# Optimization experiments

Measured on AMD Instinct MI355X. Metric: run time of the kernel, lower is better.

## Reference

```python
import jax, jax.numpy as jnp
import numpy as np

D_MODEL = 4096
D_FIBER = 16
D_CONTROL = 64
EMA_MOMENTUM = 0.9


def setup_inputs() -> dict:
    key = jax.random.key(0)
    k_h, k_f, k_w1, k_w2 = jax.random.split(key, 4)
    B, S = 4, 2048
    hidden = jax.random.normal(k_h, (B, S, D_MODEL), dtype=jnp.float32)
    # torch nn.Linear stores weight as [out, in]; fiber_proj init: normal std=0.02
    W_fiber = jax.random.normal(k_f, (D_FIBER, D_MODEL), dtype=jnp.float32) * 0.02
    # predictor[0]: Linear(d_model+d_fiber, d_control) with default torch init (uniform)
    fan_in1 = D_MODEL + D_FIBER
    bound1 = 1.0 / np.sqrt(fan_in1)
    W1 = jax.random.uniform(k_w1, (D_CONTROL, fan_in1), dtype=jnp.float32, minval=-bound1, maxval=bound1)
    b1 = jnp.zeros((D_CONTROL,), dtype=jnp.float32)
    # predictor[-2]: Linear(d_control, 1), weight normal std=0.01, bias zero
    W2 = jax.random.normal(k_w2, (1, D_CONTROL), dtype=jnp.float32) * 0.01
    b2 = jnp.zeros((1,), dtype=jnp.float32)
    lam = jnp.asarray(1.0, dtype=jnp.float32)
    return {"hidden": hidden, "W_fiber": W_fiber, "W1": W1, "b1": b1, "W2": W2, "b2": b2, "lam": lam}


def _causal_ema(delta_h, alpha):
    # h_t = alpha*h_{t-1} + (1-alpha)*d_t, h_{-1} = 0. delta_h: [B,S]
    B = delta_h.shape[0]
    def step(h_prev, d_t):
        h_t = alpha * h_prev + (1.0 - alpha) * d_t
        return h_t, h_t
    _, hs = jax.lax.scan(step, jnp.zeros((B,), delta_h.dtype), jnp.swapaxes(delta_h, 0, 1))
    return jnp.swapaxes(hs, 0, 1)  # [B,S]


def reference(hidden, W_fiber, W1, b1, W2, b2, lam):
    h = hidden.astype(jnp.float32)                      # [B,S,D]
    fiber = jnp.einsum('bsd,fd->bsf', h, W_fiber)       # [B,S,16]
    combined = jnp.concatenate([h, fiber], axis=-1)     # [B,S,D+16]
    z = jax.nn.gelu(jnp.einsum('bsc,kc->bsk', combined, W1) + b1, approximate=False)
    delta_h = jax.nn.softplus(jnp.einsum('bsk,ok->bso', z, W2) + b2)[..., 0]  # [B,S]
    field = _causal_ema(delta_h, EMA_MOMENTUM)          # [B,S]
    gate = jax.nn.sigmoid(-lam * field)
    return gate.astype(hidden.dtype), field.astype(hidden.dtype), delta_h.mean()
```

## Files before the change

kernel.cpp:

```cpp
#include <hip/hip_runtime.h>
#include <hip/hip_bf16.h>

#define D_MODEL 4096
#define NTOK    8192
#define SEQ     2048
#define RS      264

typedef short bf16x8 __attribute__((ext_vector_type(8)));
typedef float f32x4  __attribute__((ext_vector_type(4)));

typedef const __attribute__((address_space(1))) char* gas1_t;
typedef __attribute__((address_space(3))) char* las3_t;

__device__ inline void async16(const void* g, void* l) {
  __builtin_amdgcn_global_load_lds((gas1_t)g, (las3_t)l, 16, 0, 0);
}

__device__ inline short f2bf(float x) {
  __hip_bfloat16 h = __float2bfloat16(x);
  return *reinterpret_cast<short*>(&h);
}
__device__ inline float bf2f(const void* p, size_t i) {
  return __bfloat162float(((const __hip_bfloat16*)p)[i]);
}

__global__ __launch_bounds__(320) void sniff_k(const void* hid, const void* wf,
                                               const void* w1, const void* w2,
                                               const void* b1, const void* b2,
                                               const void* lam,
                                               int* flags, float* scal) {
  int wv = threadIdx.x >> 6, lane = threadIdx.x & 63;
  const unsigned short* p = nullptr;
  int n = 0;
  switch (wv) {
    case 0: p = (const unsigned short*)hid; n = NTOK * D_MODEL; break;
    case 1: p = (const unsigned short*)wf;  n = 16 * D_MODEL;   break;
    case 2: p = (const unsigned short*)w1;  n = 64 * 4112;      break;
    case 3: p = (const unsigned short*)w2;  n = 64;             break;
    case 4: p = (const unsigned short*)b1;  n = 64;             break;
  }
  int S = n / 2 < 64 ? n / 2 : 64;
  bool act = lane < S;
  unsigned short ve = 0, vo = 0;
  if (act) { ve = p[2 * lane]; vo = p[2 * lane + 1]; }
  int ee = (ve >> 7) & 0xFF, eo = (vo >> 7) & 0xFF;
  bool ve_band   = (ve == 0) || (ve == 0x8000) || (ee >= 96 && ee <= 141);
  bool vo_bandnz = (vo != 0) && (vo != 0x8000) && (eo >= 96 && eo <= 141);
  int zp = __popcll(__ballot(act && ve == 0 && vo == 0));
  int ob = __popcll(__ballot(act && ve == 0 && vo_bandnz));
  int eb = __popcll(__ballot(act && ve_band));
  if (lane == 0) {
    int f;
    if (zp == S) f = 1;
    else if (4 * ob >= 3 * S) f = 0;
    else if (4 * eb >= 3 * S) f = 1;
    else f = 0;
    flags[wv] = f;
  }
  if (threadIdx.x == 0) {
    unsigned short l0 = *(const unsigned short*)lam;
    int le = (l0 >> 7) & 0xFF;
    if (l0 != 0 && l0 != 0x8000 && le >= 96 && le <= 141)
      scal[0] = __bfloat162float(*(const __hip_bfloat16*)lam);
    else
      scal[0] = *(const float*)lam;
    unsigned short c0 = *(const unsigned short*)b2;
    int ce = (c0 >> 7) & 0xFF;
    if (c0 == 0) scal[1] = 0.0f;
    else if (c0 != 0x8000 && ce >= 96 && ce <= 141)
      scal[1] = __bfloat162float(*(const __hip_bfloat16*)b2);
    else
      scal[1] = *(const float*)b2;
  }
}

__global__ __launch_bounds__(256) void fold_w1(const void* __restrict__ W1v,
                                               const void* __restrict__ Wfv,
                                               const int* __restrict__ flags,
                                               __hip_bfloat16* __restrict__ W1eff) {
  int n = blockIdx.x;
  int fw1 = flags[2], fwf = flags[1];
  __shared__ float w1b[16];
  if (threadIdx.x < 16) {
    size_t idx = (size_t)n * 4112 + 4096 + threadIdx.x;
    w1b[threadIdx.x] = fw1 ? bf2f(W1v, idx) : ((const float*)W1v)[idx];
  }
  __syncthreads();
  for (int k = threadIdx.x; k < D_MODEL; k += 256) {
    size_t idx = (size_t)n * 4112 + k;
    float v = fw1 ? bf2f(W1v, idx) : ((const float*)W1v)[idx];
#pragma unroll
    for (int f = 0; f < 16; ++f) {
      size_t wi = (size_t)f * D_MODEL + k;
      float wfv = fwf ? bf2f(Wfv, wi) : ((const float*)Wfv)[wi];
      v += w1b[f] * wfv;
    }
    W1eff[(size_t)n * D_MODEL + k] = __float2bfloat16(v);
  }
}

__global__ __launch_bounds__(256) void gemm_fused(const void* __restrict__ hid,
                                                  const short* __restrict__ B_,
                                                  const void* __restrict__ b1,
                                                  const void* __restrict__ w2,
                                                  const int* __restrict__ flags,
                                                  const float* __restrict__ scal,
                                                  float* __restrict__ delta) {
  __shared__ short As[2][32 * RS];
  __shared__ short Bs[2][64 * RS];
  int t = blockIdx.x;
  int tid = threadIdx.x;
  int w = tid >> 6, lane = tid & 63;
  int m = lane & 15, kg = lane >> 4;
  int kh = w >> 1, rg = w & 1;
  bool lo = lane < 32;
  int l5 = lane & 31;
  f32x4 acc[4];
#pragma unroll
  for (int g = 0; g < 4; ++g) acc[g] = (f32x4){0.f, 0.f, 0.f, 0.f};

  auto compute = [&](const short* Asc, const short* Bsc) {
#pragma unroll
    for (int j = 0; j < 4; ++j) {
      int ko = kh * 128 + j * 32 + kg * 8;
      bf16x8 a   = *(const bf16x8*)(Asc + (rg * 16 + m) * RS + ko);
      bf16x8 b0v = *(const bf16x8*)(Bsc + (m +  0) * RS + ko);
      bf16x8 b1v = *(const bf16x8*)(Bsc + (m + 16) * RS + ko);
      bf16x8 b2v = *(const bf16x8*)(Bsc + (m + 32) * RS + ko);
      bf16x8 b3v = *(const bf16x8*)(Bsc + (m + 48) * RS + ko);
      acc[0] = __builtin_amdgcn_mfma_f32_16x16x32_bf16(a, b0v, acc[0], 0, 0, 0);
      acc[1] = __builtin_amdgcn_mfma_f32_16x16x32_bf16(a, b1v, acc[1], 0, 0, 0);
      acc[2] = __builtin_amdgcn_mfma_f32_16x16x32_bf16(a, b2v, acc[2], 0, 0, 0);
      acc[3] = __builtin_amdgcn_mfma_f32_16x16x32_bf16(a, b3v, acc[3], 0, 0, 0);
    }
  };

  if (flags[0]) {
    const short* hidA = (const short*)hid;
    auto stage = [&](int c, int p) {
#pragma unroll
      for (int i = 0; i < 8; ++i) {
        int r = w * 8 + i;
        const short* gp = hidA + (size_t)(t * 32 + r) * D_MODEL + c * 256 + l5 * 8;
        if (lo) async16(gp, &As[p][r * RS]);
      }
#pragma unroll
      for (int i = 0; i < 16; ++i) {
        int r = w * 16 + i;
        const short* gp = B_ + (size_t)r * D_MODEL + c * 256 + l5 * 8;
        if (lo) async16(gp, &Bs[p][r * RS]);
      }
    };
    stage(0, 0);
#pragma unroll 1
    for (int c = 0; c < 15; ++c) {
      stage(c + 1, (c + 1) & 1);
      __builtin_amdgcn_s_waitcnt(0x4F78);
      __builtin_amdgcn_s_barrier();
      compute(As[c & 1], Bs[c & 1]);
      __builtin_amdgcn_s_barrier();
    }
    __builtin_amdgcn_s_waitcnt(0x0F70);
    __builtin_amdgcn_s_barrier();
    compute(As[1], Bs[1]);
  } else {
    const float* hidF = (const float*)hid;
#pragma unroll 1
    for (int c = 0; c < 16; ++c) {
#pragma unroll
      for (int i = 0; i < 16; ++i) {
        int r = w * 16 + i;
        const short* gp = B_ + (size_t)r * D_MODEL + c * 256 + l5 * 8;
        if (lo) async16(gp, &Bs[0][r * RS]);
      }
      for (int e = tid; e < 32 * 256; e += 256) {
        int r = e >> 8, k = e & 255;
        As[0][r * RS + k] = f2bf(hidF[(size_t)(t * 32 + r) * D_MODEL + c * 256 + k]);
      }
      __syncthreads();
      compute(As[0], Bs[0]);
      __syncthreads();
    }
  }

  float* red = (float*)&As[0][0];
#pragma unroll
  for (int g = 0; g < 4; ++g)
#pragma unroll
    for (int r = 0; r < 4; ++r)
      red[kh * 2048 + (rg * 16 + kg * 4 + r) * 64 + g * 16 + m] = acc[g][r];
  __syncthreads();
  int row = tid >> 3, cid = tid & 7;
  int fb1 = flags[4], fw2 = flags[3];
  float y = 0.f;
#pragma unroll
  for (int j = 0; j < 8; ++j) {
    int col = cid + 8 * j;
    float s = red[row * 64 + col] + red[2048 + row * 64 + col];
    s += fb1 ? bf2f(b1, col) : ((const float*)b1)[col];
    float gg = 0.5f * s * (1.0f + erff(s * 0.70710678118654752f));
    y += gg * (fw2 ? bf2f(w2, col) : ((const float*)w2)[col]);
  }
#pragma unroll
  for (int off = 1; off <= 4; off <<= 1) y += __shfl_xor(y, off, 64);
  if (cid == 0) {
    float x = y + scal[1];
    delta[t * 32 + row] = (x > 20.0f) ? x : log1pf(expf(x));
  }
}

__global__ __launch_bounds__(256) void ema_out(const float* __restrict__ delta,
                                               const float* __restrict__ scal,
                                               float* __restrict__ out) {
  int b    = threadIdx.x >> 6;
  int lane = threadIdx.x & 63;
  const float alpha = 0.9f;
  float d[32];
  const float* dp = delta + b * SEQ + lane * 32;
  float beta = 0.f, lsum = 0.f;
#pragma unroll
  for (int i = 0; i < 32; ++i) {
    d[i] = dp[i];
    lsum += d[i];
    beta = alpha * beta + 0.1f * d[i];
  }
  float accA = 0.03433683820292512f;
  float accB = beta;
  for (int off = 1; off < 64; off <<= 1) {
    float uA = __shfl_up(accA, off, 64);
    float uB = __shfl_up(accB, off, 64);
    if (lane >= off) {
      accB = accB + accA * uB;
      accA = accA * uA;
    }
  }
  float prev = __shfl_up(accB, 1, 64);
  float h = (lane == 0) ? 0.f : prev;
  float lam = scal[0];
#pragma unroll
  for (int i = 0; i < 32; ++i) {
    h = alpha * h + 0.1f * d[i];
    float gate = 1.0f / (1.0f + expf(lam * h));
    out[b * SEQ + lane * 32 + i]        = gate;
    out[NTOK + b * SEQ + lane * 32 + i] = h;
  }
#pragma unroll
  for (int off = 32; off >= 1; off >>= 1) lsum += __shfl_xor(lsum, off, 64);
  __shared__ float bs[4];
  if (lane == 0) bs[b] = lsum;
  __syncthreads();
  if (threadIdx.x == 0)
    out[2 * NTOK] = (bs[0] + bs[1] + bs[2] + bs[3]) * (1.0f / 8192.0f);
}

extern "C" void kernel_launch(void* const* d_in, const int* in_sizes, int n_in,
                              void* d_out, int out_size, void* d_ws, size_t ws_size,
                              hipStream_t stream) {
  const void* hidden = d_in[0];
  const void* Wf     = d_in[1];
  const void* W1     = d_in[2];
  const void* b1     = d_in[3];
  const void* W2     = d_in[4];
  const void* b2     = d_in[5];
  const void* lam    = d_in[6];
  float* out = (float*)d_out;

  char* ws = (char*)d_ws;
  int*   flags = (int*)ws;
  float* scal  = (float*)(ws + 32);
  __hip_bfloat16* W1eff = (__hip_bfloat16*)(ws + 64);
  float* delta = (float*)(ws + 64 + (size_t)64 * D_MODEL * 2);

  sniff_k<<<1, 320, 0, stream>>>(hidden, Wf, W1, W2, b1, b2, lam, flags, scal);
  fold_w1<<<64, 256, 0, stream>>>(W1, Wf, flags, W1eff);
  gemm_fused<<<256, 256, 0, stream>>>(hidden, (const short*)W1eff, b1, W2, flags, scal, delta);
  ema_out<<<1, 256, 0, stream>>>(delta, scal, out);
}
```

Baseline: 249.5 us.

## Split GEMM K dimension across four blocks with swizzled LDS and separate epilogue

The fused GEMM is split into a split-K partial kernel: 1024 blocks of 512 threads, each covering a quarter of K. Each block writes its partial 64-wide sums to workspace. A new small kernel reduces the partials and applies bias, GELU, the W2 dot product and softplus. LDS uses an XOR-swizzled layout without padding in place of the padded stride, and double buffering is dropped in favour of higher occupancy. This raises parallelism on a 256-CU device where only one block per CU ran before, at the cost of an extra launch and partial-sum traffic.

```diff
diff --git a/kernel.cpp b/kernel.cpp
--- a/kernel.cpp
+++ b/kernel.cpp
@@ -4,7 +4,6 @@
 #define D_MODEL 4096
 #define NTOK    8192
 #define SEQ     2048
-#define RS      264
 
 typedef short bf16x8 __attribute__((ext_vector_type(8)));
 typedef float f32x4  __attribute__((ext_vector_type(4)));
@@ -99,113 +98,116 @@
   }
 }
 
-__global__ __launch_bounds__(256) void gemm_fused(const void* __restrict__ hid,
-                                                  const short* __restrict__ B_,
-                                                  const void* __restrict__ b1,
-                                                  const void* __restrict__ w2,
-                                                  const int* __restrict__ flags,
-                                                  const float* __restrict__ scal,
-                                                  float* __restrict__ delta) {
-  __shared__ short As[2][32 * RS];
-  __shared__ short Bs[2][64 * RS];
-  int t = blockIdx.x;
+__global__ __launch_bounds__(512, 6) void gemm_part(const void* __restrict__ hid,
+                                                    const short* __restrict__ B_,
+                                                    const int* __restrict__ flags,
+                                                    float* __restrict__ part) {
+  __shared__ short SMEM[24576];
+  short* As = SMEM;
+  short* Bs = SMEM + 8192;
+  int t = blockIdx.x >> 2;
+  int q = blockIdx.x & 3;
   int tid = threadIdx.x;
   int w = tid >> 6, lane = tid & 63;
   int m = lane & 15, kg = lane >> 4;
-  int kh = w >> 1, rg = w & 1;
-  bool lo = lane < 32;
-  int l5 = lane & 31;
+  int rg = w & 1, kq = w >> 1;
+  int rdma = lane >> 5;
+  int sdma = lane & 31;
   f32x4 acc[4];
 #pragma unroll
   for (int g = 0; g < 4; ++g) acc[g] = (f32x4){0.f, 0.f, 0.f, 0.f};
 
-  auto compute = [&](const short* Asc, const short* Bsc) {
-#pragma unroll
-    for (int j = 0; j < 4; ++j) {
-      int ko = kh * 128 + j * 32 + kg * 8;
-      bf16x8 a   = *(const bf16x8*)(Asc + (rg * 16 + m) * RS + ko);
-      bf16x8 b0v = *(const bf16x8*)(Bsc + (m +  0) * RS + ko);
-      bf16x8 b1v = *(const bf16x8*)(Bsc + (m + 16) * RS + ko);
-      bf16x8 b2v = *(const bf16x8*)(Bsc + (m + 32) * RS + ko);
-      bf16x8 b3v = *(const bf16x8*)(Bsc + (m + 48) * RS + ko);
+  const short* hidA = (const short*)hid;
+  int fhid = flags[0];
+
+#pragma unroll 1
+  for (int c = 0; c < 4; ++c) {
+    int kbase = q * 1024 + c * 256;
+    if (fhid) {
+#pragma unroll
+      for (int i = 0; i < 2; ++i) {
+        int r0 = w * 4 + i * 2;
+        int r  = r0 + rdma;
+        const short* gp = hidA + (size_t)(t * 32 + r) * D_MODEL + kbase +
+                          ((sdma ^ (r & 7)) * 8);
+        async16(gp, As + r0 * 256);
+      }
+    } else {
+      for (int e = tid; e < 32 * 256; e += 512) {
+        int r = e >> 8, k = e & 255;
+        float v = ((const float*)hid)[(size_t)(t * 32 + r) * D_MODEL + kbase + k];
+        As[r * 256 + (((k >> 3) ^ (r & 7)) * 8) + (k & 7)] = f2bf(v);
+      }
+    }
+#pragma unroll
+    for (int i = 0; i < 4; ++i) {
+      int r0 = w * 8 + i * 2;
+      int r  = r0 + rdma;
+      const short* gp = B_ + (size_t)r * D_MODEL + kbase + ((sdma ^ (r & 7)) * 8);
+      async16(gp, Bs + r0 * 256);
+    }
+    __syncthreads();
+#pragma unroll
+    for (int j = 0; j < 2; ++j) {
+      int sl  = kq * 8 + j * 4 + kg;
+      int off = ((sl ^ (m & 7)) * 8);
+      bf16x8 a   = *(const bf16x8*)(As + (rg * 16 + m) * 256 + off);
+      bf16x8 b0v = *(const bf16x8*)(Bs + (m +  0) * 256 + off);
+      bf16x8 b1v = *(const bf16x8*)(Bs + (m + 16) * 256 + off);
+      bf16x8 b2v = *(const bf16x8*)(Bs + (m + 32) * 256 + off);
+      bf16x8 b3v = *(const bf16x8*)(Bs + (m + 48) * 256 + off);
       acc[0] = __builtin_amdgcn_mfma_f32_16x16x32_bf16(a, b0v, acc[0], 0, 0, 0);
       acc[1] = __builtin_amdgcn_mfma_f32_16x16x32_bf16(a, b1v, acc[1], 0, 0, 0);
       acc[2] = __builtin_amdgcn_mfma_f32_16x16x32_bf16(a, b2v, acc[2], 0, 0, 0);
       acc[3] = __builtin_amdgcn_mfma_f32_16x16x32_bf16(a, b3v, acc[3], 0, 0, 0);
     }
-  };
-
-  if (flags[0]) {
-    const short* hidA = (const short*)hid;
-    auto stage = [&](int c, int p) {
-#pragma unroll
-      for (int i = 0; i < 8; ++i) {
-        int r = w * 8 + i;
-        const short* gp = hidA + (size_t)(t * 32 + r) * D_MODEL + c * 256 + l5 * 8;
-        if (lo) async16(gp, &As[p][r * RS]);
-      }
-#pragma unroll
-      for (int i = 0; i < 16; ++i) {
-        int r = w * 16 + i;
-        const short* gp = B_ + (size_t)r * D_MODEL + c * 256 + l5 * 8;
-        if (lo) async16(gp, &Bs[p][r * RS]);
-      }
-    };
-    stage(0, 0);
-#pragma unroll 1
-    for (int c = 0; c < 15; ++c) {
-      stage(c + 1, (c + 1) & 1);
-      __builtin_amdgcn_s_waitcnt(0x4F78);
-      __builtin_amdgcn_s_barrier();
-      compute(As[c & 1], Bs[c & 1]);
-      __builtin_amdgcn_s_barrier();
-    }
-    __builtin_amdgcn_s_waitcnt(0x0F70);
-    __builtin_amdgcn_s_barrier();
-    compute(As[1], Bs[1]);
-  } else {
-    const float* hidF = (const float*)hid;
-#pragma unroll 1
-    for (int c = 0; c < 16; ++c) {
-#pragma unroll
-      for (int i = 0; i < 16; ++i) {
-        int r = w * 16 + i;
-        const short* gp = B_ + (size_t)r * D_MODEL + c * 256 + l5 * 8;
-        if (lo) async16(gp, &Bs[0][r * RS]);
-      }
-      for (int e = tid; e < 32 * 256; e += 256) {
-        int r = e >> 8, k = e & 255;
-        As[0][r * RS + k] = f2bf(hidF[(size_t)(t * 32 + r) * D_MODEL + c * 256 + k]);
-      }
-      __syncthreads();
-      compute(As[0], Bs[0]);
-      __syncthreads();
-    }
-  }
-
-  float* red = (float*)&As[0][0];
+    __syncthreads();
+  }
+
+  float* red = (float*)SMEM;
 #pragma unroll
   for (int g = 0; g < 4; ++g)
 #pragma unroll
     for (int r = 0; r < 4; ++r)
-      red[kh * 2048 + (rg * 16 + kg * 4 + r) * 64 + g * 16 + m] = acc[g][r];
+      red[((kq * 32) + (rg * 16 + kg * 4 + r)) * 64 + (g * 16 + m)] = acc[g][r];
   __syncthreads();
-  int row = tid >> 3, cid = tid & 7;
+  int row = tid >> 4, cid = tid & 15;
+  float* po = part + ((size_t)q * NTOK + (size_t)t * 32 + row) * 64;
+#pragma unroll
+  for (int j = 0; j < 4; ++j) {
+    int col = cid + 16 * j;
+    float s = red[(0 * 32 + row) * 64 + col] + red[(1 * 32 + row) * 64 + col] +
+              red[(2 * 32 + row) * 64 + col] + red[(3 * 32 + row) * 64 + col];
+    po[col] = s;
+  }
+}
+
+__global__ __launch_bounds__(256) void delta_ep(const float* __restrict__ part,
+                                                const void* __restrict__ b1,
+                                                const void* __restrict__ w2,
+                                                const int* __restrict__ flags,
+                                                const float* __restrict__ scal,
+                                                float* __restrict__ delta) {
+  int tok = blockIdx.x * 16 + (threadIdx.x >> 4);
+  int cid = threadIdx.x & 15;
   int fb1 = flags[4], fw2 = flags[3];
   float y = 0.f;
 #pragma unroll
-  for (int j = 0; j < 8; ++j) {
-    int col = cid + 8 * j;
-    float s = red[row * 64 + col] + red[2048 + row * 64 + col];
+  for (int j = 0; j < 4; ++j) {
+    int col = cid + 16 * j;
+    float s = 0.f;
+#pragma unroll
+    for (int c = 0; c < 4; ++c)
+      s += part[((size_t)c * NTOK + tok) * 64 + col];
     s += fb1 ? bf2f(b1, col) : ((const float*)b1)[col];
-    float gg = 0.5f * s * (1.0f + erff(s * 0.70710678118654752f));
-    y += gg * (fw2 ? bf2f(w2, col) : ((const float*)w2)[col]);
-  }
-#pragma unroll
-  for (int off = 1; off <= 4; off <<= 1) y += __shfl_xor(y, off, 64);
+    float g = 0.5f * s * (1.0f + erff(s * 0.70710678118654752f));
+    y += g * (fw2 ? bf2f(w2, col) : ((const float*)w2)[col]);
+  }
+#pragma unroll
+  for (int off = 1; off <= 8; off <<= 1) y += __shfl_xor(y, off, 64);
   if (cid == 0) {
     float x = y + scal[1];
-    delta[t * 32 + row] = (x > 20.0f) ? x : log1pf(expf(x));
+    delta[tok] = (x > 20.0f) ? x : log1pf(expf(x));
   }
 }
 
@@ -270,9 +272,11 @@
   float* scal  = (float*)(ws + 32);
   __hip_bfloat16* W1eff = (__hip_bfloat16*)(ws + 64);
   float* delta = (float*)(ws + 64 + (size_t)64 * D_MODEL * 2);
+  float* part  = (float*)(ws + 64 + (size_t)64 * D_MODEL * 2 + NTOK * 4);
 
   sniff_k<<<1, 320, 0, stream>>>(hidden, Wf, W1, W2, b1, b2, lam, flags, scal);
   fold_w1<<<64, 256, 0, stream>>>(W1, Wf, flags, W1eff);
-  gemm_fused<<<256, 256, 0, stream>>>(hidden, (const short*)W1eff, b1, W2, flags, scal, delta);
+  gemm_part<<<1024, 512, 0, stream>>>(hidden, (const short*)W1eff, flags, part);
+  delta_ep<<<512, 256, 0, stream>>>(part, b1, W2, flags, scal, delta);
   ema_out<<<1, 256, 0, stream>>>(delta, scal, out);
 }
```

After: 262.5 us. 5.2% more time.
